# Optimization experiments

Hardware: AMD Instinct MI355X
Metric: run time of the kernel (lower is better)

The kernel has to match this reference:

```python
import jax, jax.numpy as jnp
import numpy as np

N = 50000   # nodes per branch
E = 500000  # edges per branch
B = 256     # graphs per batch
F = 320     # node feature dim = num_features_xd*10
H = 10      # GAT heads
C = 32      # GAT out channels per head
NEG_SLOPE = 0.2


def _seg_sum(x, idx, n):
    return jax.ops.segment_sum(x, idx, num_segments=n)


def gcn_conv(x, edge_index, W, b):
    n = x.shape[0]
    h = x @ W  # [N, F]
    loop = jnp.arange(n, dtype=edge_index.dtype)
    src = jnp.concatenate([edge_index[0], loop])
    dst = jnp.concatenate([edge_index[1], loop])
    deg = _seg_sum(jnp.ones_like(dst, dtype=h.dtype), dst, n)
    dinv = jnp.where(deg > 0, jax.lax.rsqrt(deg), 0.0)
    coef = (dinv[src] * dinv[dst])[:, None]  # [E+N, 1]
    out = _seg_sum(h[src] * coef, dst, n)
    return out + b


def gat_conv(x, edge_index, W, att_src, att_dst, b):
    # PyG GATConv, heads=H, concat=True, add_self_loops=True, negative_slope=0.2
    n = x.shape[0]
    h = (x @ W).reshape(n, H, C)  # [N, H, C]
    a_s = jnp.sum(h * att_src, axis=-1)  # [N, H]
    a_d = jnp.sum(h * att_dst, axis=-1)  # [N, H]
    loop = jnp.arange(n, dtype=edge_index.dtype)
    src = jnp.concatenate([edge_index[0], loop])
    dst = jnp.concatenate([edge_index[1], loop])
    e = jax.nn.leaky_relu(a_s[src] + a_d[dst], NEG_SLOPE)  # [E+N, H]
    m = jax.ops.segment_max(e, dst, num_segments=n)  # neighborhood max per head
    p = jnp.exp(e - m[dst])
    denom = _seg_sum(p, dst, n)  # [N, H], >0 thanks to self loops
    alpha = p / denom[dst]
    out = _seg_sum(h[src] * alpha[:, :, None], dst, n)  # [N, H, C]
    return out.reshape(n, H * C) + b


def graph_branch(x, edge_index, batch, params):
    x = jax.nn.relu(gcn_conv(x, edge_index, params['W_gcn'], params['b_gcn']))
    x = jax.nn.relu(gat_conv(x, edge_index, params['W_gat'], params['att_src'], params['att_dst'], params['b_gat']))
    gmp = jax.ops.segment_max(x, batch, num_segments=B)  # [B, F]
    cnt = _seg_sum(jnp.ones((x.shape[0], 1), x.dtype), batch, B)
    gap = _seg_sum(x, batch, B) / jnp.maximum(cnt, 1.0)
    g = jnp.concatenate([gmp, gap], axis=1)  # [B, 2F]
    g = jax.nn.relu(g @ params['W_fc_g1'] + params['b_fc_g1'])
    # dropout is identity in eval mode
    g = g @ params['W_fc_g2'] + params['b_fc_g2']
    return g


def _forward(x_a, x_b, edge_index_a, edge_index_b, batch_a, batch_b, params):
    ga = graph_branch(x_a, edge_index_a, batch_a, params)
    gb = graph_branch(x_b, edge_index_b, batch_b, params)
    xc = jnp.concatenate([ga, gb], axis=1)  # [B, 256]
    xc = jax.nn.relu(xc @ params['W_fc1'] + params['b_fc1'])
    xc = jax.nn.relu(xc @ params['W_fc2'] + params['b_fc2'])
    return xc @ params['W_out'] + params['b_out']  # [B, 2]


def setup_inputs() -> dict:
    key = jax.random.key(0)
    ks = jax.random.split(key, 24)
    s = 0.05
    d = {
        'x_a': jax.random.normal(ks[0], (N, F), jnp.float32),
        'x_b': jax.random.normal(ks[1], (N, F), jnp.float32),
        'edge_index_a': jax.random.randint(ks[2], (2, E), 0, N, jnp.int32),
        'edge_index_b': jax.random.randint(ks[3], (2, E), 0, N, jnp.int32),
        'batch_a': jnp.sort(jax.random.randint(ks[4], (N,), 0, B, jnp.int32)),
        'batch_b': jnp.sort(jax.random.randint(ks[5], (N,), 0, B, jnp.int32)),
        'W_gcn': jax.random.normal(ks[6], (F, F), jnp.float32) * s,
        'b_gcn': jax.random.normal(ks[7], (F,), jnp.float32) * s,
        'W_gat': jax.random.normal(ks[8], (F, H * C), jnp.float32) * s,
        'att_src': jax.random.normal(ks[9], (H, C), jnp.float32) * s,
        'att_dst': jax.random.normal(ks[10], (H, C), jnp.float32) * s,
        'b_gat': jax.random.normal(ks[11], (H * C,), jnp.float32) * s,
        'W_fc_g1': jax.random.normal(ks[12], (2 * F, 1500), jnp.float32) * s,
        'b_fc_g1': jax.random.normal(ks[13], (1500,), jnp.float32) * s,
        'W_fc_g2': jax.random.normal(ks[14], (1500, 128), jnp.float32) * s,
        'b_fc_g2': jax.random.normal(ks[15], (128,), jnp.float32) * s,
        'W_fc1': jax.random.normal(ks[16], (256, 1024), jnp.float32) * s,
        'b_fc1': jax.random.normal(ks[17], (1024,), jnp.float32) * s,
        'W_fc2': jax.random.normal(ks[18], (1024, 512), jnp.float32) * s,
        'b_fc2': jax.random.normal(ks[19], (512,), jnp.float32) * s,
        'W_out': jax.random.normal(ks[20], (512, 2), jnp.float32) * s,
        'b_out': jax.random.normal(ks[21], (2,), jnp.float32) * s,
    }
    return d


def reference(x_a, x_b, edge_index_a, edge_index_b, batch_a, batch_b,
              W_gcn, b_gcn, W_gat, att_src, att_dst, b_gat,
              W_fc_g1, b_fc_g1, W_fc_g2, b_fc_g2,
              W_fc1, b_fc1, W_fc2, b_fc2, W_out, b_out):
    params = dict(W_gcn=W_gcn, b_gcn=b_gcn, W_gat=W_gat, att_src=att_src,
                  att_dst=att_dst, b_gat=b_gat, W_fc_g1=W_fc_g1, b_fc_g1=b_fc_g1,
                  W_fc_g2=W_fc_g2, b_fc_g2=b_fc_g2, W_fc1=W_fc1, b_fc1=b_fc1,
                  W_fc2=W_fc2, b_fc2=b_fc2, W_out=W_out, b_out=b_out)
    return _forward(x_a, x_b, edge_index_a, edge_index_b, batch_a, batch_b, params)
```

## Files before the change

kernel.cpp:

```cpp
#include <hip/hip_runtime.h>
#include <type_traits>

#define FDIM 320
#define NHEADS 10
#define NGR 256

typedef __bf16 bf16x8 __attribute__((ext_vector_type(8)));
typedef float f32x4 __attribute__((ext_vector_type(4)));

__global__ void wconv2_kernel(const float* __restrict__ Wg, const float* __restrict__ Wa,
                              __bf16* __restrict__ Tg, __bf16* __restrict__ Ta) {
  int idx = blockIdx.x * 256 + threadIdx.x;
  bool first = idx < FDIM * FDIM;
  const float* W = first ? Wg : Wa;
  __bf16* T = first ? Tg : Ta;
  int i2 = first ? idx : idx - FDIM * FDIM;
  int k = i2 / FDIM, c = i2 - k * FDIM;
  T[c * FDIM + k] = (__bf16)W[i2];
}

#define GLSTR 40

template<typename TA, bool SCORES>
__global__ __launch_bounds__(256, 2) void gemm320v3_kernel(
    const TA* __restrict__ A, const __bf16* __restrict__ Wt,
    __bf16* __restrict__ C, int M,
    const float* __restrict__ att_s, const float* __restrict__ att_d,
    float* __restrict__ as_, float* __restrict__ ad_)
{
  __shared__ __bf16 As[2][64 * GLSTR];
  __shared__ __bf16 Bs[2][320 * GLSTR];

  const int tid = threadIdx.x;
  const int lane = tid & 63;
  const int w = tid >> 6;
  const int wr = w >> 1, wc = w & 1;
  const int r = lane & 15, kg = lane >> 4;
  const int m0 = blockIdx.x * 64;

  const int brow = tid >> 2, bq = tid & 3;
  const int gmrow = m0 + brow;
  const bool arow_ok = gmrow < M;

  bf16x8 bstg[5];
  bf16x8 astg;
  float4 af32a, af32b;

  auto stage_load = [&](int k0) {
    #pragma unroll
    for (int i = 0; i < 5; i++) {
      int ch = tid + i * 256;
      int col = ch >> 2, kc = ch & 3;
      bstg[i] = *(const bf16x8*)(Wt + (size_t)col * FDIM + k0 + kc * 8);
    }
    if constexpr (std::is_same_v<TA, float>) {
      if (arow_ok) {
        const float4* ap = (const float4*)(A + (size_t)gmrow * FDIM + k0 + bq * 8);
        af32a = ap[0]; af32b = ap[1];
      }
    } else {
      if (arow_ok) astg = *(const bf16x8*)(A + (size_t)gmrow * FDIM + k0 + bq * 8);
    }
  };
  auto stage_write = [&](int b) {
    #pragma unroll
    for (int i = 0; i < 5; i++) {
      int ch = tid + i * 256;
      int col = ch >> 2, kc = ch & 3;
      *(bf16x8*)&Bs[b][col * GLSTR + kc * 8] = bstg[i];
    }
    bf16x8 v = {};
    if constexpr (std::is_same_v<TA, float>) {
      if (arow_ok) {
        v[0]=(__bf16)af32a.x; v[1]=(__bf16)af32a.y; v[2]=(__bf16)af32a.z; v[3]=(__bf16)af32a.w;
        v[4]=(__bf16)af32b.x; v[5]=(__bf16)af32b.y; v[6]=(__bf16)af32b.z; v[7]=(__bf16)af32b.w;
      }
    } else {
      if (arow_ok) v = astg;
    }
    *(bf16x8*)&As[b][brow * GLSTR + bq * 8] = v;
  };

  f32x4 acc0[10], acc1[10];
  #pragma unroll
  for (int i = 0; i < 10; i++) { acc0[i] = (f32x4){0,0,0,0}; acc1[i] = (f32x4){0,0,0,0}; }

  stage_load(0);
  stage_write(0);
  __syncthreads();

  int cur = 0;
  for (int k = 0; k < 10; k++) {
    if (k < 9) stage_load((k + 1) * 32);
    {
      bf16x8 a0 = *(const bf16x8*)&As[cur][(wr*32 + r)      * GLSTR + kg*8];
      bf16x8 a1 = *(const bf16x8*)&As[cur][(wr*32 + 16 + r) * GLSTR + kg*8];
      #pragma unroll
      for (int nf = 0; nf < 10; nf++) {
        bf16x8 b = *(const bf16x8*)&Bs[cur][(wc*160 + nf*16 + r) * GLSTR + kg*8];
        acc0[nf] = __builtin_amdgcn_mfma_f32_16x16x32_bf16(a0, b, acc0[nf], 0, 0, 0);
        acc1[nf] = __builtin_amdgcn_mfma_f32_16x16x32_bf16(a1, b, acc1[nf], 0, 0, 0);
      }
    }
    if (k < 9) {
      stage_write(cur ^ 1);
      __syncthreads();
      cur ^= 1;
    }
  }

  #pragma unroll
  for (int nf = 0; nf < 10; nf++) {
    int gn = wc*160 + nf*16 + r;
    #pragma unroll
    for (int q = 0; q < 4; q++) {
      int gm0 = m0 + wr*32 + kg*4 + q;
      if (gm0 < M)       C[(size_t)gm0 * FDIM + gn] = (__bf16)acc0[nf][q];
      int gm1 = gm0 + 16;
      if (gm1 < M)       C[(size_t)gm1 * FDIM + gn] = (__bf16)acc1[nf][q];
    }
  }

  if constexpr (SCORES) {
    #pragma unroll
    for (int th = 0; th < 5; th++) {
      int t = wc * 5 + th;
      float s0 = att_s[t*32 + r],      s1 = att_s[t*32 + 16 + r];
      float d0 = att_d[t*32 + r],      d1 = att_d[t*32 + 16 + r];
      #pragma unroll
      for (int q = 0; q < 4; q++) {
        float ps0 = acc0[2*th][q]*s0 + acc0[2*th+1][q]*s1;
        float ps1 = acc1[2*th][q]*s0 + acc1[2*th+1][q]*s1;
        float pd0 = acc0[2*th][q]*d0 + acc0[2*th+1][q]*d1;
        float pd1 = acc1[2*th][q]*d0 + acc1[2*th+1][q]*d1;
        #pragma unroll
        for (int off = 1; off < 16; off <<= 1) {
          ps0 += __shfl_xor(ps0, off, 16);
          ps1 += __shfl_xor(ps1, off, 16);
          pd0 += __shfl_xor(pd0, off, 16);
          pd1 += __shfl_xor(pd1, off, 16);
        }
        if (r == 0) {
          int row0 = m0 + wr*32 + kg*4 + q;
          if (row0 < M) { as_[row0*NHEADS + t] = ps0; ad_[row0*NHEADS + t] = pd0; }
          int row1 = row0 + 16;
          if (row1 < M) { as_[row1*NHEADS + t] = ps1; ad_[row1*NHEADS + t] = pd1; }
        }
      }
    }
  }
}

#define BM 128
#define BN 64
#define BK 32
#define LSTR 56

template<int FLAGS>
__global__ __launch_bounds__(256) void gemm_bf16_kernel(
    const float* __restrict__ A, const float* __restrict__ B,
    float* __restrict__ C, const float* __restrict__ bias,
    int M, int N, int K, int ldc)
{
  __shared__ __bf16 As[BM * LSTR];
  __shared__ __bf16 Bs[BN * LSTR];

  const int tid = threadIdx.x;
  const int lane = tid & 63;
  const int w = tid >> 6;
  const int wm = w >> 1, wn = w & 1;
  const int r = lane & 15, kg = lane >> 4;
  const int m0 = blockIdx.x * BM, n0 = blockIdx.y * BN;

  f32x4 acc[4][2];
  #pragma unroll
  for (int i = 0; i < 4; i++)
    #pragma unroll
    for (int j = 0; j < 2; j++)
      acc[i][j] = (f32x4){0.f, 0.f, 0.f, 0.f};

  const int arow = tid >> 1, ahalf = tid & 1;
  const int bk = tid >> 3, bn = (tid & 7) * 8;

  for (int k0 = 0; k0 < K; k0 += BK) {
    __syncthreads();
    {
      int gm = m0 + arow;
      int kbase = k0 + ahalf * 16;
      float tmp[16];
      if (gm < M && kbase + 16 <= K) {
        const float4* ap = (const float4*)(A + (size_t)gm * K + kbase);
        #pragma unroll
        for (int q = 0; q < 4; q++) {
          float4 v = ap[q];
          tmp[q*4+0] = v.x; tmp[q*4+1] = v.y; tmp[q*4+2] = v.z; tmp[q*4+3] = v.w;
        }
      } else {
        #pragma unroll
        for (int q = 0; q < 16; q++) {
          int kk = kbase + q;
          tmp[q] = (gm < M && kk < K) ? A[(size_t)gm * K + kk] : 0.f;
        }
      }
      bf16x8 v0, v1;
      #pragma unroll
      for (int q = 0; q < 8; q++) { v0[q] = (__bf16)tmp[q]; v1[q] = (__bf16)tmp[q+8]; }
      bf16x8* dp = (bf16x8*)&As[arow * LSTR + ahalf * 16];
      dp[0] = v0; dp[1] = v1;
    }
    {
      int gk = k0 + bk;
      float tb[8];
      if (gk < K && n0 + bn + 8 <= N) {
        const float4* bp = (const float4*)(B + (size_t)gk * N + n0 + bn);
        float4 u0 = bp[0], u1 = bp[1];
        tb[0]=u0.x; tb[1]=u0.y; tb[2]=u0.z; tb[3]=u0.w;
        tb[4]=u1.x; tb[5]=u1.y; tb[6]=u1.z; tb[7]=u1.w;
      } else {
        #pragma unroll
        for (int q = 0; q < 8; q++) {
          int gn = n0 + bn + q;
          tb[q] = (gk < K && gn < N) ? B[(size_t)gk * N + gn] : 0.f;
        }
      }
      #pragma unroll
      for (int q = 0; q < 8; q++) Bs[(bn + q) * LSTR + bk] = (__bf16)tb[q];
    }
    __syncthreads();
    bf16x8 af[4], bfr[2];
    #pragma unroll
    for (int mf = 0; mf < 4; mf++)
      af[mf] = *(const bf16x8*)&As[(wm*64 + mf*16 + r) * LSTR + kg*8];
    #pragma unroll
    for (int nf = 0; nf < 2; nf++)
      bfr[nf] = *(const bf16x8*)&Bs[(wn*32 + nf*16 + r) * LSTR + kg*8];
    #pragma unroll
    for (int mf = 0; mf < 4; mf++)
      #pragma unroll
      for (int nf = 0; nf < 2; nf++)
        acc[mf][nf] = __builtin_amdgcn_mfma_f32_16x16x32_bf16(af[mf], bfr[nf], acc[mf][nf], 0, 0, 0);
  }

  #pragma unroll
  for (int mf = 0; mf < 4; mf++) {
    #pragma unroll
    for (int nf = 0; nf < 2; nf++) {
      #pragma unroll
      for (int q = 0; q < 4; q++) {
        int gm = m0 + wm*64 + mf*16 + kg*4 + q;
        int gn = n0 + wn*32 + nf*16 + r;
        if (gm < M && gn < N) {
          float v = acc[mf][nf][q];
          if (FLAGS & 2) v += bias[gn];
          if (FLAGS & 1) v = fmaxf(v, 0.f);
          C[(size_t)gm * ldc + gn] = v;
        }
      }
    }
  }
}

__global__ __launch_bounds__(256) void gemm_splitk_kernel(
    const float* __restrict__ A, const float* __restrict__ B,
    float* __restrict__ P, int M, int N, int K, int KS)
{
  __shared__ __bf16 As[BM * LSTR];
  __shared__ __bf16 Bs[BN * LSTR];

  const int tid = threadIdx.x;
  const int lane = tid & 63;
  const int w = tid >> 6;
  const int wm = w >> 1, wn = w & 1;
  const int r = lane & 15, kg = lane >> 4;
  const int m0 = blockIdx.x * BM, n0 = blockIdx.y * BN;
  const int kstart = blockIdx.z * KS;
  const int kend = min(K, kstart + KS);

  f32x4 acc[4][2];
  #pragma unroll
  for (int i = 0; i < 4; i++)
    #pragma unroll
    for (int j = 0; j < 2; j++)
      acc[i][j] = (f32x4){0.f, 0.f, 0.f, 0.f};

  const int arow = tid >> 1, ahalf = tid & 1;
  const int bk = tid >> 3, bn = (tid & 7) * 8;

  for (int k0 = kstart; k0 < kend; k0 += BK) {
    __syncthreads();
    {
      int gm = m0 + arow;
      int kbase = k0 + ahalf * 16;
      float tmp[16];
      if (gm < M && kbase + 16 <= kend) {
        const float4* ap = (const float4*)(A + (size_t)gm * K + kbase);
        #pragma unroll
        for (int q = 0; q < 4; q++) {
          float4 v = ap[q];
          tmp[q*4+0] = v.x; tmp[q*4+1] = v.y; tmp[q*4+2] = v.z; tmp[q*4+3] = v.w;
        }
      } else {
        #pragma unroll
        for (int q = 0; q < 16; q++) {
          int kk = kbase + q;
          tmp[q] = (gm < M && kk < kend) ? A[(size_t)gm * K + kk] : 0.f;
        }
      }
      bf16x8 v0, v1;
      #pragma unroll
      for (int q = 0; q < 8; q++) { v0[q] = (__bf16)tmp[q]; v1[q] = (__bf16)tmp[q+8]; }
      bf16x8* dp = (bf16x8*)&As[arow * LSTR + ahalf * 16];
      dp[0] = v0; dp[1] = v1;
    }
    {
      int gk = k0 + bk;
      float tb[8];
      if (gk < kend && n0 + bn + 8 <= N) {
        const float4* bp = (const float4*)(B + (size_t)gk * N + n0 + bn);
        float4 u0 = bp[0], u1 = bp[1];
        tb[0]=u0.x; tb[1]=u0.y; tb[2]=u0.z; tb[3]=u0.w;
        tb[4]=u1.x; tb[5]=u1.y; tb[6]=u1.z; tb[7]=u1.w;
      } else {
        #pragma unroll
        for (int q = 0; q < 8; q++) {
          int gn = n0 + bn + q;
          tb[q] = (gk < kend && gn < N) ? B[(size_t)gk * N + gn] : 0.f;
        }
      }
      #pragma unroll
      for (int q = 0; q < 8; q++) Bs[(bn + q) * LSTR + bk] = (__bf16)tb[q];
    }
    __syncthreads();
    bf16x8 af[4], bfr[2];
    #pragma unroll
    for (int mf = 0; mf < 4; mf++)
      af[mf] = *(const bf16x8*)&As[(wm*64 + mf*16 + r) * LSTR + kg*8];
    #pragma unroll
    for (int nf = 0; nf < 2; nf++)
      bfr[nf] = *(const bf16x8*)&Bs[(wn*32 + nf*16 + r) * LSTR + kg*8];
    #pragma unroll
    for (int mf = 0; mf < 4; mf++)
      #pragma unroll
      for (int nf = 0; nf < 2; nf++)
        acc[mf][nf] = __builtin_amdgcn_mfma_f32_16x16x32_bf16(af[mf], bfr[nf], acc[mf][nf], 0, 0, 0);
  }

  float* Pp = P + (size_t)blockIdx.z * M * N;
  #pragma unroll
  for (int mf = 0; mf < 4; mf++) {
    #pragma unroll
    for (int nf = 0; nf < 2; nf++) {
      #pragma unroll
      for (int q = 0; q < 4; q++) {
        int gm = m0 + wm*64 + mf*16 + kg*4 + q;
        int gn = n0 + wn*32 + nf*16 + r;
        if (gm < M && gn < N)
          Pp[(size_t)gm * N + gn] = acc[mf][nf][q];
      }
    }
  }
}

template<int FLAGS, bool STACK>
__global__ void reduce_kernel(const float* __restrict__ P, float* __restrict__ C,
                              const float* __restrict__ bias, int M, int N, int S, int ldc)
{
  int i = blockIdx.x * 256 + threadIdx.x;
  if (i >= M * N) return;
  float v = 0.f;
  for (int s = 0; s < S; s++) v += P[(size_t)s * M * N + i];
  int row = i / N, col = i - row * N;
  if (FLAGS & 2) v += bias[col];
  if (FLAGS & 1) v = fmaxf(v, 0.f);
  if (STACK) { if (row >= (M >> 1)) { row -= (M >> 1); col += N; } }
  C[(size_t)row * ldc + col] = v;
}

__global__ void count_kernel(const int* __restrict__ dst, int* __restrict__ cnt, int E) {
  int e = blockIdx.x * 256 + threadIdx.x;
  if (e < E) atomicAdd(&cnt[dst[e]], 1);
}

__global__ void bsum_kernel(const int* __restrict__ cnt, int* __restrict__ bsum, int n) {
  __shared__ int wp[4];
  int tid = threadIdx.x, lane = tid & 63, wid = tid >> 6;
  int i = blockIdx.x * 256 + tid;
  int v = (i < n) ? cnt[i] : 0;
  #pragma unroll
  for (int off = 32; off >= 1; off >>= 1) v += __shfl_xor(v, off, 64);
  if (lane == 0) wp[wid] = v;
  __syncthreads();
  if (tid == 0) bsum[blockIdx.x] = wp[0] + wp[1] + wp[2] + wp[3];
}

__global__ void bscan_kernel(int* __restrict__ bsum, int nb) {
  __shared__ int wp[4];
  int tid = threadIdx.x, lane = tid & 63, wid = tid >> 6;
  int v = (tid < nb) ? bsum[tid] : 0;
  int xv = v;
  #pragma unroll
  for (int off = 1; off < 64; off <<= 1) {
    int y = __shfl_up(xv, off, 64);
    if (lane >= off) xv += y;
  }
  if (lane == 63) wp[wid] = xv;
  __syncthreads();
  if (tid == 0) { int s = 0; for (int k = 0; k < 4; k++) { int t = wp[k]; wp[k] = s; s += t; } }
  __syncthreads();
  if (tid < nb) bsum[tid] = wp[wid] + xv - v;
}

__global__ void rpfill_kernel(const int* __restrict__ cnt, const int* __restrict__ bsum,
                              int* __restrict__ rp, float* __restrict__ dinv, int n, int E) {
  __shared__ int wp[4];
  int tid = threadIdx.x, lane = tid & 63, wid = tid >> 6;
  int i = blockIdx.x * 256 + tid;
  int v = (i < n) ? cnt[i] : 0;
  int xv = v;
  #pragma unroll
  for (int off = 1; off < 64; off <<= 1) {
    int y = __shfl_up(xv, off, 64);
    if (lane >= off) xv += y;
  }
  if (lane == 63) wp[wid] = xv;
  __syncthreads();
  if (tid == 0) { int s = 0; for (int k = 0; k < 4; k++) { int t = wp[k]; wp[k] = s; s += t; } }
  __syncthreads();
  if (i < n) {
    rp[i] = bsum[blockIdx.x] + wp[wid] + xv - v;
    dinv[i] = rsqrtf((float)(v + 1));
  }
  if (blockIdx.x == 0 && tid == 0) rp[n] = E;
}

__global__ void fill_kernel(const int* __restrict__ src, const int* __restrict__ dst,
                            const int* __restrict__ rp, int* __restrict__ fil,
                            int* __restrict__ csr, int E) {
  int e = blockIdx.x * 256 + threadIdx.x;
  if (e < E) {
    int d = dst[e];
    int pos = rp[d] + atomicAdd(&fil[d], 1);
    csr[pos] = src[e];
  }
}

__global__ void gcn_agg_kernel(const __bf16* __restrict__ h, const int* __restrict__ rp,
                               const int* __restrict__ csr, const float* __restrict__ dinv,
                               const float* __restrict__ bias, __bf16* __restrict__ out, int n)
{
  const int lane = threadIdx.x & 63;
  int v0 = blockIdx.x * 4 + (threadIdx.x >> 6);
  if (v0 >= n) return;
  const int v = __builtin_amdgcn_readfirstlane(v0);
  const bool act = lane < 40;
  const float dv = dinv[v];
  const int e0 = rp[v], e1 = rp[v + 1];
  float acc[8], bia[8];
  if (act) {
    bf16x8 hv = *(const bf16x8*)(h + (size_t)v * FDIM + 8 * lane);
    const float4* bp = (const float4*)(bias + 8 * lane);
    float4 b0 = bp[0], b1 = bp[1];
    bia[0]=b0.x; bia[1]=b0.y; bia[2]=b0.z; bia[3]=b0.w;
    bia[4]=b1.x; bia[5]=b1.y; bia[6]=b1.z; bia[7]=b1.w;
    #pragma unroll
    for (int j = 0; j < 8; j++) acc[j] = dv * (float)hv[j];
  }
  int e = e0;
  for (; e + 4 <= e1; e += 4) {
    int sj0 = csr[e], sj1 = csr[e+1], sj2 = csr[e+2], sj3 = csr[e+3];
    float c0 = dinv[sj0], c1 = dinv[sj1], c2 = dinv[sj2], c3 = dinv[sj3];
    if (act) {
      bf16x8 h0 = *(const bf16x8*)(h + (size_t)sj0 * FDIM + 8 * lane);
      bf16x8 h1 = *(const bf16x8*)(h + (size_t)sj1 * FDIM + 8 * lane);
      bf16x8 h2 = *(const bf16x8*)(h + (size_t)sj2 * FDIM + 8 * lane);
      bf16x8 h3 = *(const bf16x8*)(h + (size_t)sj3 * FDIM + 8 * lane);
      #pragma unroll
      for (int j = 0; j < 8; j++)
        acc[j] += c0 * (float)h0[j] + c1 * (float)h1[j]
                + c2 * (float)h2[j] + c3 * (float)h3[j];
    }
  }
  for (; e < e1; e++) {
    int sj = csr[e];
    float cj = dinv[sj];
    if (act) {
      bf16x8 hv = *(const bf16x8*)(h + (size_t)sj * FDIM + 8 * lane);
      #pragma unroll
      for (int j = 0; j < 8; j++) acc[j] += cj * (float)hv[j];
    }
  }
  if (act) {
    bf16x8 o;
    #pragma unroll
    for (int j = 0; j < 8; j++) o[j] = (__bf16)fmaxf(dv * acc[j] + bia[j], 0.f);
    *(bf16x8*)(out + (size_t)v * FDIM + 8 * lane) = o;
  }
}

__device__ __forceinline__ float lrelu(float x) { return x > 0.f ? x : 0.2f * x; }

__global__ void mdenom4_kernel(const int* __restrict__ rp, const int* __restrict__ csr,
                               const float* __restrict__ as_, const float* __restrict__ ad_,
                               float* __restrict__ aint, float* __restrict__ aself, int n)
{
  int tid = blockIdx.x * 256 + threadIdx.x;
  if (tid >= n * NHEADS) return;
  int v = tid / NHEADS, t = tid - v * NHEADS;
  int e0 = rp[v], e1 = rp[v + 1];
  float adv = ad_[tid];
  float esf = lrelu(as_[tid] + adv);
  float m = esf, den = 1.f;
  for (int e = e0; e < e1; e++) {
    int s = csr[e];
    float ev = lrelu(as_[s * NHEADS + t] + adv);
    float nm = fmaxf(m, ev);
    den = den * __expf(m - nm) + __expf(ev - nm);
    m = nm;
  }
  float inv = 1.f / den;
  for (int e = e0; e < e1; e++) {
    int s = csr[e];
    aint[(size_t)e * NHEADS + t] = __expf(lrelu(as_[s * NHEADS + t] + adv) - m) * inv;
  }
  aself[tid] = __expf(esf - m) * inv;
}

__global__ void gat_agg_kernel(const __bf16* __restrict__ h, const int* __restrict__ rp,
                               const int* __restrict__ csr, const float* __restrict__ aint,
                               const float* __restrict__ aself, const float* __restrict__ bias,
                               __bf16* __restrict__ out, int n)
{
  const int lane = threadIdx.x & 63;
  int v0 = blockIdx.x * 4 + (threadIdx.x >> 6);
  if (v0 >= n) return;
  const int v = __builtin_amdgcn_readfirstlane(v0);
  const bool act = lane < 40;
  const int hl = lane >> 2;
  const int e0 = rp[v], e1 = rp[v + 1];

  float acc[8], bia[8];
  if (act) {
    float aslf = aself[v * NHEADS + hl];
    bf16x8 hv = *(const bf16x8*)(h + (size_t)v * FDIM + 8 * lane);
    const float4* bp = (const float4*)(bias + 8 * lane);
    float4 b0 = bp[0], b1 = bp[1];
    bia[0]=b0.x; bia[1]=b0.y; bia[2]=b0.z; bia[3]=b0.w;
    bia[4]=b1.x; bia[5]=b1.y; bia[6]=b1.z; bia[7]=b1.w;
    #pragma unroll
    for (int j = 0; j < 8; j++) acc[j] = aslf * (float)hv[j];
  }

  int e = e0;
  for (; e + 4 <= e1; e += 4) {
    int sj0 = csr[e], sj1 = csr[e+1], sj2 = csr[e+2], sj3 = csr[e+3];
    if (act) {
      float a0 = aint[(size_t)(e+0) * NHEADS + hl];
      float a1 = aint[(size_t)(e+1) * NHEADS + hl];
      float a2 = aint[(size_t)(e+2) * NHEADS + hl];
      float a3 = aint[(size_t)(e+3) * NHEADS + hl];
      bf16x8 h0 = *(const bf16x8*)(h + (size_t)sj0 * FDIM + 8 * lane);
      bf16x8 h1 = *(const bf16x8*)(h + (size_t)sj1 * FDIM + 8 * lane);
      bf16x8 h2 = *(const bf16x8*)(h + (size_t)sj2 * FDIM + 8 * lane);
      bf16x8 h3 = *(const bf16x8*)(h + (size_t)sj3 * FDIM + 8 * lane);
      #pragma unroll
      for (int j = 0; j < 8; j++)
        acc[j] += a0 * (float)h0[j] + a1 * (float)h1[j]
                + a2 * (float)h2[j] + a3 * (float)h3[j];
    }
  }
  for (; e < e1; e++) {
    int sj = csr[e];
    if (act) {
      float al = aint[(size_t)e * NHEADS + hl];
      bf16x8 hv = *(const bf16x8*)(h + (size_t)sj * FDIM + 8 * lane);
      #pragma unroll
      for (int j = 0; j < 8; j++) acc[j] += al * (float)hv[j];
    }
  }
  if (act) {
    bf16x8 o;
    #pragma unroll
    for (int j = 0; j < 8; j++) o[j] = (__bf16)fmaxf(acc[j] + bia[j], 0.f);
    *(bf16x8*)(out + (size_t)v * FDIM + 8 * lane) = o;
  }
}

__global__ void bstart_kernel(const int* __restrict__ batch, int* __restrict__ bstart,
                              int n, int B_) {
  int v = blockIdx.x * 256 + threadIdx.x;
  if (v > n) return;
  int bv = (v < n) ? batch[v] : B_;
  int bp = (v == 0) ? -1 : batch[v - 1];
  for (int gg = bp + 1; gg <= bv; gg++) bstart[gg] = v;
}

__global__ __launch_bounds__(256) void pool_kernel(
    const __bf16* __restrict__ xin, const int* __restrict__ bstart,
    float* __restrict__ g)
{
  __shared__ float pmx[4][FDIM];
  __shared__ float psm[4][FDIM];
  const int gid = blockIdx.x;
  const int lane = threadIdx.x & 63;
  const int wid = threadIdx.x >> 6;
  const bool act = lane < 40;
  const int s = bstart[gid], e = bstart[gid + 1];
  float mx[8], sm[8];
  #pragma unroll
  for (int j = 0; j < 8; j++) { mx[j] = -__builtin_inff(); sm[j] = 0.f; }
  for (int v = s + wid; v < e; v += 4) {
    if (act) {
      bf16x8 hv = *(const bf16x8*)(xin + (size_t)v * FDIM + 8 * lane);
      #pragma unroll
      for (int j = 0; j < 8; j++) {
        float val = (float)hv[j];
        mx[j] = fmaxf(mx[j], val);
        sm[j] += val;
      }
    }
  }
  if (act) {
    #pragma unroll
    for (int j = 0; j < 8; j++) {
      pmx[wid][8 * lane + j] = mx[j];
      psm[wid][8 * lane + j] = sm[j];
    }
  }
  __syncthreads();
  if (wid == 0 && act) {
    float cntf = (float)(e - s);
    float rcnt = 1.f / fmaxf(cntf, 1.f);
    #pragma unroll
    for (int j = 0; j < 8; j++) {
      int c = 8 * lane + j;
      float m2 = fmaxf(fmaxf(pmx[0][c], pmx[1][c]), fmaxf(pmx[2][c], pmx[3][c]));
      float s2 = psm[0][c] + psm[1][c] + psm[2][c] + psm[3][c];
      g[gid * (2 * FDIM) + c] = m2;
      g[gid * (2 * FDIM) + FDIM + c] = s2 * rcnt;
    }
  }
}

extern "C" void kernel_launch(void* const* d_in, const int* in_sizes, int n_in,
                              void* d_out, int out_size, void* d_ws, size_t ws_size,
                              hipStream_t stream)
{
  const int N = in_sizes[0] / FDIM;
  const int E = in_sizes[2] / 2;
  const int NB = (N + 255) / 256;

  const float* x[2]   = {(const float*)d_in[0], (const float*)d_in[1]};
  const int*   ei[2]  = {(const int*)d_in[2], (const int*)d_in[3]};
  const int*   bat[2] = {(const int*)d_in[4], (const int*)d_in[5]};
  const float* W_gcn   = (const float*)d_in[6];
  const float* b_gcn   = (const float*)d_in[7];
  const float* W_gat   = (const float*)d_in[8];
  const float* att_src = (const float*)d_in[9];
  const float* att_dst = (const float*)d_in[10];
  const float* b_gat   = (const float*)d_in[11];
  const float* W_fc_g1 = (const float*)d_in[12];
  const float* b_fc_g1 = (const float*)d_in[13];
  const float* W_fc_g2 = (const float*)d_in[14];
  const float* b_fc_g2 = (const float*)d_in[15];
  const float* W_fc1   = (const float*)d_in[16];
  const float* b_fc1   = (const float*)d_in[17];
  const float* W_fc2   = (const float*)d_in[18];
  const float* b_fc2   = (const float*)d_in[19];
  const float* W_out   = (const float*)d_in[20];
  const float* b_out   = (const float*)d_in[21];
  float* outp = (float*)d_out;

  char* ws = (char*)d_ws;
  size_t off = 0;
  auto alloc = [&](size_t bytes) -> char* {
    char* p = ws + off;
    off += (bytes + 255) & ~(size_t)255;
    return p;
  };
  int*    cnt    = (int*)alloc((size_t)N * 4);
  int*    fil    = (int*)alloc((size_t)N * 4);
  size_t  zero_span = (size_t)((char*)fil - (char*)cnt) + ((size_t)N * 4 + 255 & ~(size_t)255);
  int*    rp     = (int*)alloc((size_t)(N + 1) * 4);
  int*    bsum   = (int*)alloc((size_t)NB * 4);
  int*    csr    = (int*)alloc((size_t)E * 4);
  float*  dinv   = (float*)alloc((size_t)N * 4);
  int*    bstart = (int*)alloc((size_t)(NGR + 1) * 4);
  __bf16* WgcnT  = (__bf16*)alloc((size_t)FDIM * FDIM * 2);
  __bf16* WgatT  = (__bf16*)alloc((size_t)FDIM * FDIM * 2);
  __bf16* hbuf   = (__bf16*)alloc((size_t)N * FDIM * 2);
  __bf16* xbuf   = (__bf16*)alloc((size_t)N * FDIM * 2);
  float*  as_    = (float*)alloc((size_t)N * NHEADS * 4);
  float*  ad_    = (float*)alloc((size_t)N * NHEADS * 4);
  float*  aint   = (float*)alloc((size_t)E * NHEADS * 4);
  float*  aself  = (float*)alloc((size_t)N * NHEADS * 4);
  float*  g      = (float*)alloc((size_t)2 * NGR * 2 * FDIM * 4);
  float*  t1     = (float*)alloc((size_t)2 * NGR * 1500 * 4);
  float*  xc     = (float*)alloc((size_t)NGR * 256 * 4);
  float*  t2     = (float*)alloc((size_t)NGR * 1024 * 4);
  float*  t3     = (float*)alloc((size_t)NGR * 512 * 4);
  float*  part   = (float*)alloc((size_t)8 * 512 * 512 * 4);
  if (off > ws_size) return;

  wconv2_kernel<<<2 * (FDIM * FDIM) / 256, 256, 0, stream>>>(W_gcn, W_gat, WgcnT, WgatT);

  for (int br = 0; br < 2; br++) {
    hipMemsetAsync(cnt, 0, zero_span, stream);
    const int* srcp = ei[br];
    const int* dstp = ei[br] + E;
    count_kernel<<<(E + 255) / 256, 256, 0, stream>>>(dstp, cnt, E);
    bsum_kernel<<<NB, 256, 0, stream>>>(cnt, bsum, N);
    bscan_kernel<<<1, 256, 0, stream>>>(bsum, NB);
    rpfill_kernel<<<NB, 256, 0, stream>>>(cnt, bsum, rp, dinv, N, E);
    fill_kernel<<<(E + 255) / 256, 256, 0, stream>>>(srcp, dstp, rp, fil, csr, E);

    int g320 = (N + 63) / 64;
    gemm320v3_kernel<float, false><<<g320, 256, 0, stream>>>(
        x[br], WgcnT, hbuf, N, nullptr, nullptr, nullptr, nullptr);
    gcn_agg_kernel<<<(N + 3) / 4, 256, 0, stream>>>(hbuf, rp, csr, dinv, b_gcn, xbuf, N);
    gemm320v3_kernel<__bf16, true><<<g320, 256, 0, stream>>>(
        xbuf, WgatT, hbuf, N, att_src, att_dst, as_, ad_);

    mdenom4_kernel<<<(N * NHEADS + 255) / 256, 256, 0, stream>>>(rp, csr, as_, ad_, aint, aself, N);
    gat_agg_kernel<<<(N + 3) / 4, 256, 0, stream>>>(hbuf, rp, csr, aint, aself, b_gat, xbuf, N);

    bstart_kernel<<<(N + 256) / 256, 256, 0, stream>>>(bat[br], bstart, N, NGR);
    pool_kernel<<<NGR, 256, 0, stream>>>(xbuf, bstart, g + (size_t)br * NGR * 2 * FDIM);
  }

  {
    dim3 gfc1((512 + BM - 1) / BM, (1500 + BN - 1) / BN);
    gemm_bf16_kernel<3><<<gfc1, 256, 0, stream>>>(g, W_fc_g1, t1, b_fc_g1, 512, 1500, 2 * FDIM, 1500);
    int S = 8, KS = ((1500 + S * BK - 1) / (S * BK)) * BK;
    dim3 gfc2((512 + BM - 1) / BM, (128 + BN - 1) / BN, S);
    gemm_splitk_kernel<<<gfc2, 256, 0, stream>>>(t1, W_fc_g2, part, 512, 128, 1500, KS);
    reduce_kernel<2, true><<<(512 * 128 + 255) / 256, 256, 0, stream>>>(part, xc, b_fc_g2, 512, 128, S, 256);
  }
  {
    dim3 gx1((NGR + BM - 1) / BM, (1024 + BN - 1) / BN);
    gemm_bf16_kernel<3><<<gx1, 256, 0, stream>>>(xc, W_fc1, t2, b_fc1, NGR, 1024, 256, 1024);
    int S = 4, KS = ((1024 + S * BK - 1) / (S * BK)) * BK;
    dim3 gx2((NGR + BM - 1) / BM, (512 + BN - 1) / BN, S);
    gemm_splitk_kernel<<<gx2, 256, 0, stream>>>(t2, W_fc2, part, NGR, 512, 1024, KS);
    reduce_kernel<3, false><<<(NGR * 512 + 255) / 256, 256, 0, stream>>>(part, t3, b_fc2, NGR, 512, S, 512);
    int S2 = 4, KS2 = ((512 + S2 * BK - 1) / (S2 * BK)) * BK;
    dim3 gx3((NGR + BM - 1) / BM, 1, S2);
    gemm_splitk_kernel<<<gx3, 256, 0, stream>>>(t3, W_out, part, NGR, 2, 512, KS2);
    reduce_kernel<2, false><<<(NGR * 2 + 255) / 256, 256, 0, stream>>>(part, outp, b_out, NGR, 2, S2, 2);
  }
}
```

Measured before the change: 655.9 us.

## Batch both graph branches into single kernel launches with padded node offsets

Both graph branches are merged into one combined graph, with branch B's nodes offset by a padded count, so each CSR build, GEMM, aggregation and pooling kernel launches once over twice the work instead of twice per branch. This halves the number of launches and gives each kernel a larger grid to fill the GPU. The scan kernel grows to 1024 threads to cover the doubled block count, and the attention-intermediate buffer is aliased with the split-K partial buffer to save workspace. The risks are the bookkeeping for padded rows and the assumption that the doubled block count fits in one 1024-thread scan.

New measurement: 612.1 us. -6.7%, faster.

```diff
diff --git a/kernel.cpp b/kernel.cpp
--- a/kernel.cpp
+++ b/kernel.cpp
@@ -23,8 +23,8 @@
 
 template<typename TA, bool SCORES>
 __global__ __launch_bounds__(256, 2) void gemm320v3_kernel(
-    const TA* __restrict__ A, const __bf16* __restrict__ Wt,
-    __bf16* __restrict__ C, int M,
+    const TA* __restrict__ A, const TA* __restrict__ A2, int Npad, int Nreal,
+    const __bf16* __restrict__ Wt, __bf16* __restrict__ C,
     const float* __restrict__ att_s, const float* __restrict__ att_d,
     float* __restrict__ as_, float* __restrict__ ad_)
 {
@@ -37,10 +37,13 @@
   const int wr = w >> 1, wc = w & 1;
   const int r = lane & 15, kg = lane >> 4;
   const int m0 = blockIdx.x * 64;
+  const bool brB = m0 >= Npad;
+  const int loff = brB ? Npad : 0;
 
   const int brow = tid >> 2, bq = tid & 3;
-  const int gmrow = m0 + brow;
-  const bool arow_ok = gmrow < M;
+  const int grow = m0 + brow;
+  const int lrow = grow - loff;
+  const bool arow_ok = lrow < Nreal;
 
   bf16x8 bstg[5];
   bf16x8 astg;
@@ -55,11 +58,12 @@
     }
     if constexpr (std::is_same_v<TA, float>) {
       if (arow_ok) {
-        const float4* ap = (const float4*)(A + (size_t)gmrow * FDIM + k0 + bq * 8);
+        const float* Ab = brB ? A2 : A;
+        const float4* ap = (const float4*)(Ab + (size_t)lrow * FDIM + k0 + bq * 8);
         af32a = ap[0]; af32b = ap[1];
       }
     } else {
-      if (arow_ok) astg = *(const bf16x8*)(A + (size_t)gmrow * FDIM + k0 + bq * 8);
+      if (arow_ok) astg = *(const bf16x8*)(A + (size_t)grow * FDIM + k0 + bq * 8);
     }
   };
   auto stage_write = [&](int b) {
@@ -115,9 +119,9 @@
     #pragma unroll
     for (int q = 0; q < 4; q++) {
       int gm0 = m0 + wr*32 + kg*4 + q;
-      if (gm0 < M)       C[(size_t)gm0 * FDIM + gn] = (__bf16)acc0[nf][q];
+      if (gm0 - loff < Nreal) C[(size_t)gm0 * FDIM + gn] = (__bf16)acc0[nf][q];
       int gm1 = gm0 + 16;
-      if (gm1 < M)       C[(size_t)gm1 * FDIM + gn] = (__bf16)acc1[nf][q];
+      if (gm1 - loff < Nreal) C[(size_t)gm1 * FDIM + gn] = (__bf16)acc1[nf][q];
     }
   }
 
@@ -142,9 +146,9 @@
         }
         if (r == 0) {
           int row0 = m0 + wr*32 + kg*4 + q;
-          if (row0 < M) { as_[row0*NHEADS + t] = ps0; ad_[row0*NHEADS + t] = pd0; }
+          if (row0 - loff < Nreal) { as_[row0*NHEADS + t] = ps0; ad_[row0*NHEADS + t] = pd0; }
           int row1 = row0 + 16;
-          if (row1 < M) { as_[row1*NHEADS + t] = ps1; ad_[row1*NHEADS + t] = pd1; }
+          if (row1 - loff < Nreal) { as_[row1*NHEADS + t] = ps1; ad_[row1*NHEADS + t] = pd1; }
         }
       }
     }
@@ -376,9 +380,11 @@
   C[(size_t)row * ldc + col] = v;
 }
 
-__global__ void count_kernel(const int* __restrict__ dst, int* __restrict__ cnt, int E) {
+__global__ void count_kernel(const int* __restrict__ dst_a, const int* __restrict__ dst_b,
+                             int* __restrict__ cnt, int E, int Npad) {
   int e = blockIdx.x * 256 + threadIdx.x;
-  if (e < E) atomicAdd(&cnt[dst[e]], 1);
+  if (e < E) atomicAdd(&cnt[dst_a[e]], 1);
+  else if (e < 2 * E) atomicAdd(&cnt[dst_b[e - E] + Npad], 1);
 }
 
 __global__ void bsum_kernel(const int* __restrict__ cnt, int* __restrict__ bsum, int n) {
@@ -393,8 +399,8 @@
   if (tid == 0) bsum[blockIdx.x] = wp[0] + wp[1] + wp[2] + wp[3];
 }
 
-__global__ void bscan_kernel(int* __restrict__ bsum, int nb) {
-  __shared__ int wp[4];
+__global__ __launch_bounds__(1024) void bscan_kernel(int* __restrict__ bsum, int nb) {
+  __shared__ int wp[16];
   int tid = threadIdx.x, lane = tid & 63, wid = tid >> 6;
   int v = (tid < nb) ? bsum[tid] : 0;
   int xv = v;
@@ -405,13 +411,13 @@
   }
   if (lane == 63) wp[wid] = xv;
   __syncthreads();
-  if (tid == 0) { int s = 0; for (int k = 0; k < 4; k++) { int t = wp[k]; wp[k] = s; s += t; } }
+  if (tid == 0) { int s = 0; for (int k = 0; k < 16; k++) { int t = wp[k]; wp[k] = s; s += t; } }
   __syncthreads();
   if (tid < nb) bsum[tid] = wp[wid] + xv - v;
 }
 
 __global__ void rpfill_kernel(const int* __restrict__ cnt, const int* __restrict__ bsum,
-                              int* __restrict__ rp, float* __restrict__ dinv, int n, int E) {
+                              int* __restrict__ rp, float* __restrict__ dinv, int n, int E2) {
   __shared__ int wp[4];
   int tid = threadIdx.x, lane = tid & 63, wid = tid >> 6;
   int i = blockIdx.x * 256 + tid;
@@ -430,28 +436,33 @@
     rp[i] = bsum[blockIdx.x] + wp[wid] + xv - v;
     dinv[i] = rsqrtf((float)(v + 1));
   }
-  if (blockIdx.x == 0 && tid == 0) rp[n] = E;
-}
-
-__global__ void fill_kernel(const int* __restrict__ src, const int* __restrict__ dst,
+  if (blockIdx.x == 0 && tid == 0) rp[n] = E2;
+}
+
+__global__ void fill_kernel(const int* __restrict__ sa, const int* __restrict__ da,
+                            const int* __restrict__ sb, const int* __restrict__ db,
                             const int* __restrict__ rp, int* __restrict__ fil,
-                            int* __restrict__ csr, int E) {
+                            int* __restrict__ csr, int E, int Npad) {
   int e = blockIdx.x * 256 + threadIdx.x;
-  if (e < E) {
-    int d = dst[e];
-    int pos = rp[d] + atomicAdd(&fil[d], 1);
-    csr[pos] = src[e];
-  }
+  if (e >= 2 * E) return;
+  int s, d;
+  if (e < E) { s = sa[e]; d = da[e]; }
+  else       { s = sb[e - E] + Npad; d = db[e - E] + Npad; }
+  int pos = rp[d] + atomicAdd(&fil[d], 1);
+  csr[pos] = s;
 }
 
 __global__ void gcn_agg_kernel(const __bf16* __restrict__ h, const int* __restrict__ rp,
                                const int* __restrict__ csr, const float* __restrict__ dinv,
-                               const float* __restrict__ bias, __bf16* __restrict__ out, int n)
+                               const float* __restrict__ bias, __bf16* __restrict__ out,
+                               int n2, int Npad, int Nreal)
 {
   const int lane = threadIdx.x & 63;
   int v0 = blockIdx.x * 4 + (threadIdx.x >> 6);
-  if (v0 >= n) return;
+  if (v0 >= n2) return;
   const int v = __builtin_amdgcn_readfirstlane(v0);
+  const int lv = (v >= Npad) ? v - Npad : v;
+  if (lv >= Nreal) return;
   const bool act = lane < 40;
   const float dv = dinv[v];
   const int e0 = rp[v], e1 = rp[v + 1];
@@ -501,11 +512,14 @@
 
 __global__ void mdenom4_kernel(const int* __restrict__ rp, const int* __restrict__ csr,
                                const float* __restrict__ as_, const float* __restrict__ ad_,
-                               float* __restrict__ aint, float* __restrict__ aself, int n)
+                               float* __restrict__ aint, float* __restrict__ aself,
+                               int n2, int Npad, int Nreal)
 {
   int tid = blockIdx.x * 256 + threadIdx.x;
-  if (tid >= n * NHEADS) return;
+  if (tid >= n2 * NHEADS) return;
   int v = tid / NHEADS, t = tid - v * NHEADS;
+  int lv = (v >= Npad) ? v - Npad : v;
+  if (lv >= Nreal) return;
   int e0 = rp[v], e1 = rp[v + 1];
   float adv = ad_[tid];
   float esf = lrelu(as_[tid] + adv);
@@ -528,12 +542,14 @@
 __global__ void gat_agg_kernel(const __bf16* __restrict__ h, const int* __restrict__ rp,
                                const int* __restrict__ csr, const float* __restrict__ aint,
                                const float* __restrict__ aself, const float* __restrict__ bias,
-                               __bf16* __restrict__ out, int n)
+                               __bf16* __restrict__ out, int n2, int Npad, int Nreal)
 {
   const int lane = threadIdx.x & 63;
   int v0 = blockIdx.x * 4 + (threadIdx.x >> 6);
-  if (v0 >= n) return;
+  if (v0 >= n2) return;
   const int v = __builtin_amdgcn_readfirstlane(v0);
+  const int lv = (v >= Npad) ? v - Npad : v;
+  if (lv >= Nreal) return;
   const bool act = lane < 40;
   const int hl = lane >> 2;
   const int e0 = rp[v], e1 = rp[v + 1];
@@ -585,13 +601,18 @@
   }
 }
 
-__global__ void bstart_kernel(const int* __restrict__ batch, int* __restrict__ bstart,
-                              int n, int B_) {
-  int v = blockIdx.x * 256 + threadIdx.x;
-  if (v > n) return;
-  int bv = (v < n) ? batch[v] : B_;
+__global__ void bstart_kernel(const int* __restrict__ ba, const int* __restrict__ bb,
+                              int* __restrict__ bst, int n, int Npad) {
+  int idx = blockIdx.x * 256 + threadIdx.x;
+  if (idx >= 2 * (n + 1)) return;
+  int br = idx >= (n + 1);
+  int v = idx - br * (n + 1);
+  const int* batch = br ? bb : ba;
+  int off = br ? Npad : 0;
+  int* bs = bst + br * (NGR + 1);
+  int bv = (v < n) ? batch[v] : NGR;
   int bp = (v == 0) ? -1 : batch[v - 1];
-  for (int gg = bp + 1; gg <= bv; gg++) bstart[gg] = v;
+  for (int gg = bp + 1; gg <= bv; gg++) bs[gg] = v + off;
 }
 
 __global__ __launch_bounds__(256) void pool_kernel(
@@ -601,10 +622,13 @@
   __shared__ float pmx[4][FDIM];
   __shared__ float psm[4][FDIM];
   const int gid = blockIdx.x;
+  const int br = gid >= NGR;
+  const int lg = gid - br * NGR;
+  const int* bs = bstart + br * (NGR + 1);
   const int lane = threadIdx.x & 63;
   const int wid = threadIdx.x >> 6;
   const bool act = lane < 40;
-  const int s = bstart[gid], e = bstart[gid + 1];
+  const int s = bs[lg], e = bs[lg + 1];
   float mx[8], sm[8];
   #pragma unroll
   for (int j = 0; j < 8; j++) { mx[j] = -__builtin_inff(); sm[j] = 0.f; }
@@ -647,11 +671,16 @@
 {
   const int N = in_sizes[0] / FDIM;
   const int E = in_sizes[2] / 2;
-  const int NB = (N + 255) / 256;
-
-  const float* x[2]   = {(const float*)d_in[0], (const float*)d_in[1]};
-  const int*   ei[2]  = {(const int*)d_in[2], (const int*)d_in[3]};
-  const int*   bat[2] = {(const int*)d_in[4], (const int*)d_in[5]};
+  const int Npad = (N + 63) & ~63;
+  const int n2 = 2 * Npad;
+  const int NB2 = (n2 + 255) / 256;
+
+  const float* x_a = (const float*)d_in[0];
+  const float* x_b = (const float*)d_in[1];
+  const int*   ei_a = (const int*)d_in[2];
+  const int*   ei_b = (const int*)d_in[3];
+  const int*   bat_a = (const int*)d_in[4];
+  const int*   bat_b = (const int*)d_in[5];
   const float* W_gcn   = (const float*)d_in[6];
   const float* b_gcn   = (const float*)d_in[7];
   const float* W_gat   = (const float*)d_in[8];
@@ -677,55 +706,54 @@
     off += (bytes + 255) & ~(size_t)255;
     return p;
   };
-  int*    cnt    = (int*)alloc((size_t)N * 4);
-  int*    fil    = (int*)alloc((size_t)N * 4);
-  size_t  zero_span = (size_t)((char*)fil - (char*)cnt) + ((size_t)N * 4 + 255 & ~(size_t)255);
-  int*    rp     = (int*)alloc((size_t)(N + 1) * 4);
-  int*    bsum   = (int*)alloc((size_t)NB * 4);
-  int*    csr    = (int*)alloc((size_t)E * 4);
-  float*  dinv   = (float*)alloc((size_t)N * 4);
-  int*    bstart = (int*)alloc((size_t)(NGR + 1) * 4);
+  int*    cnt    = (int*)alloc((size_t)n2 * 4);
+  int*    fil    = (int*)alloc((size_t)n2 * 4);
+  size_t  zero_span = (size_t)((char*)fil - (char*)cnt) + (((size_t)n2 * 4 + 255) & ~(size_t)255);
+  int*    rp     = (int*)alloc((size_t)(n2 + 1) * 4);
+  int*    bsum   = (int*)alloc((size_t)NB2 * 4);
+  int*    csr    = (int*)alloc((size_t)2 * E * 4);
+  float*  dinv   = (float*)alloc((size_t)n2 * 4);
+  int*    bstart = (int*)alloc((size_t)2 * (NGR + 1) * 4);
   __bf16* WgcnT  = (__bf16*)alloc((size_t)FDIM * FDIM * 2);
   __bf16* WgatT  = (__bf16*)alloc((size_t)FDIM * FDIM * 2);
-  __bf16* hbuf   = (__bf16*)alloc((size_t)N * FDIM * 2);
-  __bf16* xbuf   = (__bf16*)alloc((size_t)N * FDIM * 2);
-  float*  as_    = (float*)alloc((size_t)N * NHEADS * 4);
-  float*  ad_    = (float*)alloc((size_t)N * NHEADS * 4);
-  float*  aint   = (float*)alloc((size_t)E * NHEADS * 4);
-  float*  aself  = (float*)alloc((size_t)N * NHEADS * 4);
+  __bf16* hbuf   = (__bf16*)alloc((size_t)n2 * FDIM * 2);
+  __bf16* xbuf   = (__bf16*)alloc((size_t)n2 * FDIM * 2);
+  float*  as_    = (float*)alloc((size_t)n2 * NHEADS * 4);
+  float*  ad_    = (float*)alloc((size_t)n2 * NHEADS * 4);
+  float*  aself  = (float*)alloc((size_t)n2 * NHEADS * 4);
+  size_t aint_bytes = (size_t)2 * E * NHEADS * 4;
+  size_t part_bytes = (size_t)8 * 512 * 512 * 4;
+  float*  aint   = (float*)alloc(aint_bytes > part_bytes ? aint_bytes : part_bytes);
+  float*  part   = aint;
   float*  g      = (float*)alloc((size_t)2 * NGR * 2 * FDIM * 4);
   float*  t1     = (float*)alloc((size_t)2 * NGR * 1500 * 4);
   float*  xc     = (float*)alloc((size_t)NGR * 256 * 4);
   float*  t2     = (float*)alloc((size_t)NGR * 1024 * 4);
   float*  t3     = (float*)alloc((size_t)NGR * 512 * 4);
-  float*  part   = (float*)alloc((size_t)8 * 512 * 512 * 4);
   if (off > ws_size) return;
 
   wconv2_kernel<<<2 * (FDIM * FDIM) / 256, 256, 0, stream>>>(W_gcn, W_gat, WgcnT, WgatT);
 
-  for (int br = 0; br < 2; br++) {
-    hipMemsetAsync(cnt, 0, zero_span, stream);
-    const int* srcp = ei[br];
-    const int* dstp = ei[br] + E;
-    count_kernel<<<(E + 255) / 256, 256, 0, stream>>>(dstp, cnt, E);
-    bsum_kernel<<<NB, 256, 0, stream>>>(cnt, bsum, N);
-    bscan_kernel<<<1, 256, 0, stream>>>(bsum, NB);
-    rpfill_kernel<<<NB, 256, 0, stream>>>(cnt, bsum, rp, dinv, N, E);
-    fill_kernel<<<(E + 255) / 256, 256, 0, stream>>>(srcp, dstp, rp, fil, csr, E);
-
-    int g320 = (N + 63) / 64;
-    gemm320v3_kernel<float, false><<<g320, 256, 0, stream>>>(
-        x[br], WgcnT, hbuf, N, nullptr, nullptr, nullptr, nullptr);
-    gcn_agg_kernel<<<(N + 3) / 4, 256, 0, stream>>>(hbuf, rp, csr, dinv, b_gcn, xbuf, N);
-    gemm320v3_kernel<__bf16, true><<<g320, 256, 0, stream>>>(
-        xbuf, WgatT, hbuf, N, att_src, att_dst, as_, ad_);
-
-    mdenom4_kernel<<<(N * NHEADS + 255) / 256, 256, 0, stream>>>(rp, csr, as_, ad_, aint, aself, N);
-    gat_agg_kernel<<<(N + 3) / 4, 256, 0, stream>>>(hbuf, rp, csr, aint, aself, b_gat, xbuf, N);
-
-    bstart_kernel<<<(N + 256) / 256, 256, 0, stream>>>(bat[br], bstart, N, NGR);
-    pool_kernel<<<NGR, 256, 0, stream>>>(xbuf, bstart, g + (size_t)br * NGR * 2 * FDIM);
-  }
+  hipMemsetAsync(cnt, 0, zero_span, stream);
+  count_kernel<<<(2 * E + 255) / 256, 256, 0, stream>>>(ei_a + E, ei_b + E, cnt, E, Npad);
+  bsum_kernel<<<NB2, 256, 0, stream>>>(cnt, bsum, n2);
+  bscan_kernel<<<1, 1024, 0, stream>>>(bsum, NB2);
+  rpfill_kernel<<<NB2, 256, 0, stream>>>(cnt, bsum, rp, dinv, n2, 2 * E);
+  fill_kernel<<<(2 * E + 255) / 256, 256, 0, stream>>>(ei_a, ei_a + E, ei_b, ei_b + E,
+                                                       rp, fil, csr, E, Npad);
+
+  int g320 = n2 / 64;
+  gemm320v3_kernel<float, false><<<g320, 256, 0, stream>>>(
+      x_a, x_b, Npad, N, WgcnT, hbuf, nullptr, nullptr, nullptr, nullptr);
+  gcn_agg_kernel<<<(n2 + 3) / 4, 256, 0, stream>>>(hbuf, rp, csr, dinv, b_gcn, xbuf, n2, Npad, N);
+  gemm320v3_kernel<__bf16, true><<<g320, 256, 0, stream>>>(
+      xbuf, nullptr, Npad, N, WgatT, hbuf, att_src, att_dst, as_, ad_);
+
+  mdenom4_kernel<<<(n2 * NHEADS + 255) / 256, 256, 0, stream>>>(rp, csr, as_, ad_, aint, aself, n2, Npad, N);
+  gat_agg_kernel<<<(n2 + 3) / 4, 256, 0, stream>>>(hbuf, rp, csr, aint, aself, b_gat, xbuf, n2, Npad, N);
+
+  bstart_kernel<<<(2 * (N + 1) + 255) / 256, 256, 0, stream>>>(bat_a, bat_b, bstart, N, Npad);
+  pool_kernel<<<2 * NGR, 256, 0, stream>>>(xbuf, bstart, g);
 
   {
     dim3 gfc1((512 + BM - 1) / BM, (1500 + BN - 1) / BN);
```
